# Kernel optimization log

Hardware: AMD Instinct MI355X
Metric: run time of the kernel (lower is better)

Reference implementation:

```python
import jax, jax.numpy as jnp
import numpy as np


def setup_inputs() -> dict:
    key = jax.random.key(0)
    k1, k2 = jax.random.split(key)
    N, T, D = 4096, 64, 1024
    h = jax.random.normal(k1, (N, T, D), dtype=jnp.float32)
    # nn.Linear(d_model, 1, bias=False) weight, flattened to [D]
    w_score = jax.random.normal(k2, (D,), dtype=jnp.float32) * (1.0 / np.sqrt(D))
    return {"h": h, "w_score": w_score}


def reference(h, w_score):
    # scores: [N, T] = h @ w_score  (Linear(d_model, 1, bias=False) then squeeze)
    scores = jnp.einsum('ntd,d->nt', h, w_score)
    alpha = jax.nn.softmax(scores, axis=-1)          # softmax over tokens T
    pooled = jnp.einsum('nt,ntd->nd', alpha, h)      # weighted sum pooling
    return (pooled, alpha)
```

## Files before the change

kernel.cpp:

```cpp
#include <hip/hip_runtime.h>
#include <math.h>


#define T_TOK 64
#define D_DIM 1024
#define D4 (D_DIM / 4)
#define WAVES_PER_BLOCK 4

__global__ __launch_bounds__(256) void attn_pool_kernel(
    const float* __restrict__ h,
    const float* __restrict__ w,
    float* __restrict__ pooled,
    float* __restrict__ alpha,
    int N)
{
    const int tid  = threadIdx.x;
    const int wave = tid >> 6;
    const int lane = tid & 63;
    const int n = blockIdx.x * WAVES_PER_BLOCK + wave;
    if (n >= N) return;

    const float4* __restrict__ h4 = (const float4*)(h + (size_t)n * T_TOK * D_DIM);
    const float4* __restrict__ w4 = (const float4*)w;

    float4 wf[4];
    #pragma unroll
    for (int j = 0; j < 4; ++j) wf[j] = w4[lane + 64 * j];

    float4 acc[4];
    #pragma unroll
    for (int j = 0; j < 4; ++j) acc[j] = make_float4(0.f, 0.f, 0.f, 0.f);

    float l_sum = 0.f;
    float my_e  = 0.f;

    float4 hc[4];
    #pragma unroll
    for (int j = 0; j < 4; ++j) hc[j] = h4[lane + 64 * j];

    for (int t = 0; t < T_TOK; ++t) {
        float4 hn[4];
        const bool have_next = (t + 1 < T_TOK);
        if (have_next) {
            const float4* __restrict__ row = h4 + (size_t)(t + 1) * D4;
            #pragma unroll
            for (int j = 0; j < 4; ++j) hn[j] = row[lane + 64 * j];
        }

        float s = 0.f;
        #pragma unroll
        for (int j = 0; j < 4; ++j) {
            s = fmaf(hc[j].x, wf[j].x, s);
            s = fmaf(hc[j].y, wf[j].y, s);
            s = fmaf(hc[j].z, wf[j].z, s);
            s = fmaf(hc[j].w, wf[j].w, s);
        }
        #pragma unroll
        for (int off = 32; off > 0; off >>= 1)
            s += __shfl_xor(s, off, 64);

        const float e = expf(s);
        l_sum += e;
        my_e = (lane == t) ? e : my_e;

        #pragma unroll
        for (int j = 0; j < 4; ++j) {
            acc[j].x = fmaf(e, hc[j].x, acc[j].x);
            acc[j].y = fmaf(e, hc[j].y, acc[j].y);
            acc[j].z = fmaf(e, hc[j].z, acc[j].z);
            acc[j].w = fmaf(e, hc[j].w, acc[j].w);
        }

        if (have_next) {
            #pragma unroll
            for (int j = 0; j < 4; ++j) hc[j] = hn[j];
        }
    }

    const float inv_l = 1.0f / l_sum;

    float4* __restrict__ p4 = (float4*)pooled + (size_t)n * D4;
    #pragma unroll
    for (int j = 0; j < 4; ++j) {
        float4 o;
        o.x = acc[j].x * inv_l;
        o.y = acc[j].y * inv_l;
        o.z = acc[j].z * inv_l;
        o.w = acc[j].w * inv_l;
        p4[lane + 64 * j] = o;
    }

    alpha[(size_t)n * T_TOK + lane] = my_e * inv_l;
}

extern "C" void kernel_launch(void* const* d_in, const int* in_sizes, int n_in,
                              void* d_out, int out_size, void* d_ws, size_t ws_size,
                              hipStream_t stream)
{
    const float* h = (const float*)d_in[0];
    const float* w = (const float*)d_in[1];
    const int N = in_sizes[0] / (T_TOK * D_DIM);

    float* pooled = (float*)d_out;
    float* alpha  = pooled + (size_t)N * D_DIM;

    const int blocks = (N + WAVES_PER_BLOCK - 1) / WAVES_PER_BLOCK;
    attn_pool_kernel<<<blocks, WAVES_PER_BLOCK * 64, 0, stream>>>(
        h, w, pooled, alpha, N);
}
```

Measured before the change: 1.328 ms.

## Deepen row prefetch to three ahead and use DPP wave reduction

Replaces the single-row prefetch with a four-buffer rotation that keeps two to three token rows in flight per wave, so more memory loads can hide latency. The shuffle-based reduction becomes a DPP row-shift plus row-broadcast reduction with a readlane, and expf becomes __expf. A launch-bounds minimum of four blocks is added. The extra register buffers may add pressure, and __expf is less accurate.

```diff
diff --git a/kernel.cpp b/kernel.cpp
--- a/kernel.cpp
+++ b/kernel.cpp
@@ -7,7 +7,69 @@
 #define D4 (D_DIM / 4)
 #define WAVES_PER_BLOCK 4
 
-__global__ __launch_bounds__(256) void attn_pool_kernel(
+__device__ __forceinline__ float wave_sum64(float v) {
+    int t;
+    t = __builtin_amdgcn_update_dpp(0, __float_as_int(v), 0x111, 0xf, 0xf, true);
+    v += __int_as_float(t);
+    t = __builtin_amdgcn_update_dpp(0, __float_as_int(v), 0x112, 0xf, 0xf, true);
+    v += __int_as_float(t);
+    t = __builtin_amdgcn_update_dpp(0, __float_as_int(v), 0x114, 0xf, 0xf, true);
+    v += __int_as_float(t);
+    t = __builtin_amdgcn_update_dpp(0, __float_as_int(v), 0x118, 0xf, 0xf, true);
+    v += __int_as_float(t);
+    t = __builtin_amdgcn_update_dpp(0, __float_as_int(v), 0x142, 0xf, 0xf, true);
+    v += __int_as_float(t);
+    t = __builtin_amdgcn_update_dpp(0, __float_as_int(v), 0x143, 0xf, 0xf, true);
+    v += __int_as_float(t);
+    return __int_as_float(__builtin_amdgcn_readlane(__float_as_int(v), 63));
+}
+
+__device__ __forceinline__ void load_row(float4 (&R)[4], const float4* __restrict__ h4,
+                                         int t, int lane) {
+    const float4* __restrict__ row = h4 + (size_t)t * D4;
+    R[0] = row[lane];
+    R[1] = row[lane + 64];
+    R[2] = row[lane + 128];
+    R[3] = row[lane + 192];
+}
+
+__device__ __forceinline__ void process_row(const float4 (&R)[4], const float4 (&wf)[4],
+                                            float4 (&acc)[4], float& l_sum, float& my_e,
+                                            int lane, int tk) {
+    float p0 = 0.f, p1 = 0.f, p2 = 0.f, p3 = 0.f;
+    p0 = fmaf(R[0].x, wf[0].x, p0);
+    p0 = fmaf(R[0].y, wf[0].y, p0);
+    p0 = fmaf(R[0].z, wf[0].z, p0);
+    p0 = fmaf(R[0].w, wf[0].w, p0);
+    p1 = fmaf(R[1].x, wf[1].x, p1);
+    p1 = fmaf(R[1].y, wf[1].y, p1);
+    p1 = fmaf(R[1].z, wf[1].z, p1);
+    p1 = fmaf(R[1].w, wf[1].w, p1);
+    p2 = fmaf(R[2].x, wf[2].x, p2);
+    p2 = fmaf(R[2].y, wf[2].y, p2);
+    p2 = fmaf(R[2].z, wf[2].z, p2);
+    p2 = fmaf(R[2].w, wf[2].w, p2);
+    p3 = fmaf(R[3].x, wf[3].x, p3);
+    p3 = fmaf(R[3].y, wf[3].y, p3);
+    p3 = fmaf(R[3].z, wf[3].z, p3);
+    p3 = fmaf(R[3].w, wf[3].w, p3);
+    const float s = (p0 + p1) + (p2 + p3);
+
+    const float st = wave_sum64(s);
+    const float e  = __expf(st);
+    l_sum += e;
+    my_e = (lane == tk) ? e : my_e;
+
+    #pragma unroll
+    for (int j = 0; j < 4; ++j) {
+        acc[j].x = fmaf(e, R[j].x, acc[j].x);
+        acc[j].y = fmaf(e, R[j].y, acc[j].y);
+        acc[j].z = fmaf(e, R[j].z, acc[j].z);
+        acc[j].w = fmaf(e, R[j].w, acc[j].w);
+    }
+}
+
+__global__ __launch_bounds__(256, 4) void attn_pool_kernel(
     const float* __restrict__ h,
     const float* __restrict__ w,
     float* __restrict__ pooled,
@@ -34,47 +96,22 @@
     float l_sum = 0.f;
     float my_e  = 0.f;
 
-    float4 hc[4];
-    #pragma unroll
-    for (int j = 0; j < 4; ++j) hc[j] = h4[lane + 64 * j];
+    float4 A[4], B[4], C[4], Dv[4];
+    load_row(A, h4, 0, lane);
+    load_row(B, h4, 1, lane);
 
-    for (int t = 0; t < T_TOK; ++t) {
-        float4 hn[4];
-        const bool have_next = (t + 1 < T_TOK);
-        if (have_next) {
-            const float4* __restrict__ row = h4 + (size_t)(t + 1) * D4;
-            #pragma unroll
-            for (int j = 0; j < 4; ++j) hn[j] = row[lane + 64 * j];
-        }
+    for (int t = 0; t < T_TOK; t += 4) {
+        load_row(C, h4, t + 2, lane);
+        process_row(A, wf, acc, l_sum, my_e, lane, t);
 
-        float s = 0.f;
-        #pragma unroll
-        for (int j = 0; j < 4; ++j) {
-            s = fmaf(hc[j].x, wf[j].x, s);
-            s = fmaf(hc[j].y, wf[j].y, s);
-            s = fmaf(hc[j].z, wf[j].z, s);
-            s = fmaf(hc[j].w, wf[j].w, s);
-        }
-        #pragma unroll
-        for (int off = 32; off > 0; off >>= 1)
-            s += __shfl_xor(s, off, 64);
+        load_row(Dv, h4, t + 3, lane);
+        process_row(B, wf, acc, l_sum, my_e, lane, t + 1);
 
-        const float e = expf(s);
-        l_sum += e;
-        my_e = (lane == t) ? e : my_e;
+        if (t + 4 < T_TOK) load_row(A, h4, t + 4, lane);
+        process_row(C, wf, acc, l_sum, my_e, lane, t + 2);
 
-        #pragma unroll
-        for (int j = 0; j < 4; ++j) {
-            acc[j].x = fmaf(e, hc[j].x, acc[j].x);
-            acc[j].y = fmaf(e, hc[j].y, acc[j].y);
-            acc[j].z = fmaf(e, hc[j].z, acc[j].z);
-            acc[j].w = fmaf(e, hc[j].w, acc[j].w);
-        }
-
-        if (have_next) {
-            #pragma unroll
-            for (int j = 0; j < 4; ++j) hc[j] = hn[j];
-        }
+        if (t + 5 < T_TOK) load_row(B, h4, t + 5, lane);
+        process_row(Dv, wf, acc, l_sum, my_e, lane, t + 3);
     }
 
     const float inv_l = 1.0f / l_sum;
```

After: 1.360 ms. 1.02x slower.
